# Kernel tuning notes

Hardware: AMD Instinct MI355X
Metric: run time of the kernel (lower is better)

Reference implementation:

```python
import jax, jax.numpy as jnp
import numpy as np

N_NODES = 50000


def setup_inputs() -> dict:
    key = jax.random.key(0)
    ks = jax.random.split(key, 6)
    F_IN, F_HID, N_EDGES = 128, 512, 800000
    x = jax.random.normal(ks[0], (N_NODES, F_IN), dtype=jnp.float32)
    edge_index = jax.random.randint(ks[1], (2, N_EDGES), 0, N_NODES, dtype=jnp.int64)
    W1 = jax.random.normal(ks[2], (F_IN, F_HID), dtype=jnp.float32) * (1.0 / np.sqrt(F_IN))
    b1 = jnp.zeros((F_HID,), dtype=jnp.float32)
    W2 = jax.random.normal(ks[3], (F_HID, F_IN), dtype=jnp.float32) * (1.0 / np.sqrt(F_HID))
    b2 = jnp.zeros((F_IN,), dtype=jnp.float32)
    eps = jnp.zeros((), dtype=jnp.float32)  # train_eps=True, init 0
    return {"x": x, "edge_index": edge_index, "W1": W1, "b1": b1, "W2": W2, "b2": b2, "eps": eps}


def reference(x, edge_index, W1, b1, W2, b2, eps):
    # GINConv: out = MLP((1+eps)*x + sum_{j in N(i)} x_j)
    src, dst = edge_index[0], edge_index[1]
    agg = jax.ops.segment_sum(x[src], dst, num_segments=N_NODES)  # [N, F]
    h = (1.0 + eps) * x + agg
    h = jax.nn.relu(h @ W1 + b1)
    out = h @ W2 + b2
    return out
```

## Files before the change

kernel.cpp:

```cpp
#include <hip/hip_runtime.h>
#include <hip/hip_bf16.h>

#define N_NODES 50000
#define F_IN    128
#define F_HID   512
#define N_EDGES 800000

#define NBKT 782
#define NREP 8
#define RCAP 256
#define NDMAX 64
#define NZERO 50000

typedef __bf16 bf16x2 __attribute__((ext_vector_type(2)));
typedef __bf16 bf16x4 __attribute__((ext_vector_type(4)));
typedef __bf16 bf16x8 __attribute__((ext_vector_type(8)));
typedef float  f32x4  __attribute__((ext_vector_type(4)));
typedef unsigned short u16x8 __attribute__((ext_vector_type(8)));

#define NB_E 782
__global__ __launch_bounds__(256) void fillk(const int* __restrict__ ei,
                                             int* __restrict__ bcnt,
                                             int* __restrict__ entries) {
    int b = blockIdx.x, tid = threadIdx.x;
    int e0 = (b * 256 + tid) * 4;
    int rep = b & (NREP - 1);
    if (e0 + 4 <= N_EDGES) {
        int4 s4 = *(const int4*)&ei[e0];
        int4 d4 = *(const int4*)&ei[N_EDGES + e0];
        int c0 = (d4.x >> 6) * NREP + rep;
        int c1 = (d4.y >> 6) * NREP + rep;
        int c2 = (d4.z >> 6) * NREP + rep;
        int c3 = (d4.w >> 6) * NREP + rep;
        int p0 = atomicAdd(&bcnt[c0 * 16], 1);
        int p1 = atomicAdd(&bcnt[c1 * 16], 1);
        int p2 = atomicAdd(&bcnt[c2 * 16], 1);
        int p3 = atomicAdd(&bcnt[c3 * 16], 1);
        if (p0 < RCAP) entries[(size_t)c0 * RCAP + p0] = ((d4.x & 63) << 16) | s4.x;
        if (p1 < RCAP) entries[(size_t)c1 * RCAP + p1] = ((d4.y & 63) << 16) | s4.y;
        if (p2 < RCAP) entries[(size_t)c2 * RCAP + p2] = ((d4.z & 63) << 16) | s4.z;
        if (p3 < RCAP) entries[(size_t)c3 * RCAP + p3] = ((d4.w & 63) << 16) | s4.w;
    } else {
        for (int k = 0; k < 4; ++k) {
            int e = e0 + k;
            if (e < N_EDGES) {
                int src = ei[e], dst = ei[N_EDGES + e];
                int c = (dst >> 6) * NREP + rep;
                int p = atomicAdd(&bcnt[c * 16], 1);
                if (p < RCAP) entries[(size_t)c * RCAP + p] = ((dst & 63) << 16) | src;
            }
        }
    }
}

#define NB_X 6250
#define NB_W 32
__global__ __launch_bounds__(256) void prep(const float* __restrict__ x,
                                            const float* __restrict__ W1,
                                            const float* __restrict__ W2,
                                            __bf16* __restrict__ xb,
                                            __bf16* __restrict__ w1f,
                                            __bf16* __restrict__ w2f) {
    int b = blockIdx.x, tid = threadIdx.x;
    if (b < NB_X) {
        int i = b * 256 + tid;
        float4 v = ((const float4*)x)[i];
        bf16x4 o = {(__bf16)v.x, (__bf16)v.y, (__bf16)v.z, (__bf16)v.w};
        ((bf16x4*)xb)[i] = o;
    } else if (b < NB_X + NB_W) {
        int t = (b - NB_X) * 256 + tid;
        int lane = t & 63, kk = (t >> 6) & 3, nt = (t >> 8) & 7, c = (t >> 11) & 3;
        int q = lane >> 4, l16 = lane & 15;
        bf16x8 o;
        #pragma unroll
        for (int j = 0; j < 8; ++j)
            o[j] = (__bf16)W1[(kk * 32 + q * 8 + j) * F_HID + c * 128 + nt * 16 + l16];
        *(bf16x8*)(w1f + (size_t)t * 8) = o;
    } else {
        int t = (b - NB_X - NB_W) * 256 + tid;
        int lane = t & 63, kk = (t >> 6) & 3, nt = (t >> 8) & 7, c = (t >> 11) & 3;
        int q = lane >> 4, l16 = lane & 15;
        bf16x8 o;
        #pragma unroll
        for (int j = 0; j < 8; ++j)
            o[j] = (__bf16)W2[(c * 128 + kk * 32 + q * 8 + j) * F_IN + nt * 16 + l16];
        *(bf16x8*)(w2f + (size_t)t * 8) = o;
    }
}

__global__ __launch_bounds__(512) void gin_fused(const __bf16* __restrict__ xb,
                                                 const int* __restrict__ bcnt,
                                                 const int* __restrict__ entries,
                                                 const float* __restrict__ eps,
                                                 const __bf16* __restrict__ w1f,
                                                 const __bf16* __restrict__ w2f,
                                                 const float* __restrict__ b1,
                                                 const float* __restrict__ b2,
                                                 float* __restrict__ out) {
    __shared__ union __attribute__((aligned(16))) {
        struct { int degs[64]; unsigned short bin16[64 * NDMAX]; } p0;
        __bf16 Hb[8192];
    } u;
    __shared__ __attribute__((aligned(16))) __bf16 As[8192];

    const int tid = threadIdx.x;
    const int wave = tid >> 6, lane = tid & 63;
    const int q = lane >> 4, l16 = lane & 15;
    const int bkt = blockIdx.x;

    if (tid < 64) u.p0.degs[tid] = 0;
    {
        const int zz = (NZERO << 16) | NZERO;
        int* b32 = (int*)u.p0.bin16;
        #pragma unroll
        for (int k = 0; k < 4; ++k) b32[tid * 4 + k] = zz;
    }
    __syncthreads();

    {
        int cell = bkt * NREP + wave;
        int cnt = bcnt[cell * 16];
        cnt = cnt < RCAP ? cnt : RCAP;
        const int* eb = entries + (size_t)cell * RCAP;
        for (int i = lane; i < cnt; i += 64) {
            int en = eb[i];
            int dl = en >> 16;
            int p = atomicAdd(&u.p0.degs[dl], 1);
            if (p < NDMAX)
                u.p0.bin16[dl * NDMAX + (p & 3) * 16 + (p >> 2)] =
                    (unsigned short)(en & 0xffff);
        }
    }
    __syncthreads();

    const float s = 1.0f + eps[0];
#define ROW(idx) (*(const bf16x8*)(xb + (size_t)(idx) * F_IN + l16 * 8))
    #pragma unroll 2
    for (int t = 0; t < 8; ++t) {
        int n = wave * 8 + t;
        int node = bkt * 64 + n;
        int dg = u.p0.degs[n];
        dg = dg < NDMAX ? dg : NDMAX;
        int myc = (dg + 3 - q) >> 2;
        u16x8 I0 = *(const u16x8*)&u.p0.bin16[n * NDMAX + q * 16];
        u16x8 I1 = *(const u16x8*)&u.p0.bin16[n * NDMAX + q * 16 + 8];

        float acc[8];
        #pragma unroll
        for (int i = 0; i < 8; ++i) acc[i] = 0.0f;
        if (q == 0) {
            bf16x8 self = ROW(node);
            #pragma unroll
            for (int i = 0; i < 8; ++i) acc[i] = (float)self[i] * s;
        }

        bf16x8 ra0 = ROW(I0[0]), ra1 = ROW(I0[1]), ra2 = ROW(I0[2]), ra3 = ROW(I0[3]);
        bf16x8 rb0 = ROW(I0[4]), rb1 = ROW(I0[5]), rb2 = ROW(I0[6]), rb3 = ROW(I0[7]);
        #pragma unroll
        for (int i = 0; i < 8; ++i)
            acc[i] += ((float)ra0[i] + (float)ra1[i]) + ((float)ra2[i] + (float)ra3[i]);
        #pragma unroll
        for (int i = 0; i < 8; ++i)
            acc[i] += ((float)rb0[i] + (float)rb1[i]) + ((float)rb2[i] + (float)rb3[i]);

        if (myc > 8) {
            #pragma unroll
            for (int v = 0; v < 8; ++v)
                if (myc > 8 + v) {
                    bf16x8 r = ROW(I1[v]);
                    #pragma unroll
                    for (int i = 0; i < 8; ++i) acc[i] += (float)r[i];
                }
        }

        #pragma unroll
        for (int i = 0; i < 8; ++i) {
            acc[i] += __shfl_xor(acc[i], 16);
            acc[i] += __shfl_xor(acc[i], 32);
        }
        if (lane < 16) {
            int g = n >> 4, r16 = n & 15;
            bf16x8 o;
            #pragma unroll
            for (int i = 0; i < 8; ++i) o[i] = (__bf16)acc[i];
            int byte = (g * 16 + lane) * 256 + r16 * 16;
            byte ^= (lane & 7) << 4;
            *(bf16x8*)((char*)As + byte) = o;
        }
    }
    __syncthreads();

    const int wr = wave >> 2, wc = wave & 3;

    f32x4 acc_o[2][2];
    #pragma unroll
    for (int ni = 0; ni < 2; ++ni) {
        float bv = b2[wc * 32 + ni * 16 + l16];
        f32x4 b4 = {bv, bv, bv, bv};
        acc_o[0][ni] = b4;
        acc_o[1][ni] = b4;
    }

    for (int c = 0; c < 4; ++c) {
        f32x4 acc_h[2][2];
        #pragma unroll
        for (int ni = 0; ni < 2; ++ni) {
            float bv = b1[c * 128 + wc * 32 + ni * 16 + l16];
            f32x4 b4 = {bv, bv, bv, bv};
            acc_h[0][ni] = b4;
            acc_h[1][ni] = b4;
        }
        #pragma unroll
        for (int kk = 0; kk < 4; ++kk) {
            bf16x8 am[2], bw[2];
            #pragma unroll
            for (int mi = 0; mi < 2; ++mi) {
                int g = wr * 2 + mi;
                int byte = ((g * 4 + kk) * 4 + q) * 256 + l16 * 16;
                byte ^= ((kk * 4 + q) & 7) << 4;
                am[mi] = *(const bf16x8*)((const char*)As + byte);
            }
            #pragma unroll
            for (int ni = 0; ni < 2; ++ni)
                bw[ni] = *(const bf16x8*)(w1f +
                    ((size_t)((c * 8 + wc * 2 + ni) * 4 + kk) << 9) + lane * 8);
            #pragma unroll
            for (int mi = 0; mi < 2; ++mi)
                #pragma unroll
                for (int ni = 0; ni < 2; ++ni)
                    acc_h[mi][ni] = __builtin_amdgcn_mfma_f32_16x16x32_bf16(
                        am[mi], bw[ni], acc_h[mi][ni], 0, 0, 0);
        }
        #pragma unroll
        for (int mi = 0; mi < 2; ++mi) {
            int g = wr * 2 + mi;
            #pragma unroll
            for (int ni = 0; ni < 2; ++ni)
                #pragma unroll
                for (int r = 0; r < 4; ++r)
                    u.Hb[(((g * 4 + wc) * 64 + (ni * 2 + (l16 >> 3)) * 16 + q * 4 + r) << 3)
                         + (l16 & 7)] = (__bf16)fmaxf(acc_h[mi][ni][r], 0.0f);
        }
        __syncthreads();

        #pragma unroll
        for (int kk = 0; kk < 4; ++kk) {
            bf16x8 am[2], bw[2];
            #pragma unroll
            for (int mi = 0; mi < 2; ++mi)
                am[mi] = *(const bf16x8*)&u.Hb[(((wr * 2 + mi) * 4 + kk) * 64 + lane) << 3];
            #pragma unroll
            for (int ni = 0; ni < 2; ++ni)
                bw[ni] = *(const bf16x8*)(w2f +
                    ((size_t)((c * 8 + wc * 2 + ni) * 4 + kk) << 9) + lane * 8);
            #pragma unroll
            for (int mi = 0; mi < 2; ++mi)
                #pragma unroll
                for (int ni = 0; ni < 2; ++ni)
                    acc_o[mi][ni] = __builtin_amdgcn_mfma_f32_16x16x32_bf16(
                        am[mi], bw[ni], acc_o[mi][ni], 0, 0, 0);
        }
        __syncthreads();
    }

    const int m0 = bkt * 64;
    #pragma unroll
    for (int mi = 0; mi < 2; ++mi)
        #pragma unroll
        for (int ni = 0; ni < 2; ++ni)
            #pragma unroll
            for (int r = 0; r < 4; ++r) {
                int m = m0 + wr * 32 + mi * 16 + q * 4 + r;
                if (m < N_NODES)
                    out[(size_t)m * F_IN + wc * 32 + ni * 16 + l16] = acc_o[mi][ni][r];
            }
}

extern "C" void kernel_launch(void* const* d_in, const int* in_sizes, int n_in,
                              void* d_out, int out_size, void* d_ws, size_t ws_size,
                              hipStream_t stream) {
    const float* x   = (const float*)d_in[0];
    const int*   ei  = (const int*)d_in[1];
    const float* W1  = (const float*)d_in[2];
    const float* b1  = (const float*)d_in[3];
    const float* W2  = (const float*)d_in[4];
    const float* b2  = (const float*)d_in[5];
    const float* eps = (const float*)d_in[6];
    float* out = (float*)d_out;

    char* ws = (char*)d_ws;
    __bf16* xb   = (__bf16*)ws;
    __bf16* w1f  = (__bf16*)(ws + 12900000);
    __bf16* w2f  = (__bf16*)(ws + 13100000);
    int*    bcnt = (int*)(ws + 13300000);
    int*    entries = (int*)(ws + 13800000);

    hipMemsetAsync(bcnt, 0, NBKT * NREP * 64, stream);
    hipMemsetAsync((char*)ws + (size_t)N_NODES * F_IN * 2, 0, 48 * F_IN * 2, stream);
    fillk<<<NB_E, 256, 0, stream>>>(ei, bcnt, entries);
    prep<<<NB_X + 2 * NB_W, 256, 0, stream>>>(x, W1, W2, xb, w1f, w2f);
    gin_fused<<<NBKT, 512, 0, stream>>>(xb, bcnt, entries, eps, w1f, w2f, b1, b2, out);
}
```

Baseline: 187.4 us.

## Merge fill and prep kernels; bucket edges via block-local LDS histogram

The edge-bucketing kernel and the bf16 conversion kernel become one launch with 1024-thread blocks. Each fill block first builds a per-bucket histogram in shared memory, then reserves space with a single global atomic per bucket, which replaces one global atomic per edge and the 8-way replica cells. The main kernel then reads one contiguous bucket of up to 1280 entries per block, spread across all 512 threads. This removes a launch and most of the global atomic contention. The cost is LDS atomics and extra block barriers, plus a capacity cap that could drop edges if a bucket overflows.

```diff
diff --git a/kernel.cpp b/kernel.cpp
--- a/kernel.cpp
+++ b/kernel.cpp
@@ -7,8 +7,7 @@
 #define N_EDGES 800000
 
 #define NBKT 782
-#define NREP 8
-#define RCAP 256
+#define BKCAP 1280
 #define NDMAX 64
 #define NZERO 50000
 
@@ -18,57 +17,62 @@
 typedef float  f32x4  __attribute__((ext_vector_type(4)));
 typedef unsigned short u16x8 __attribute__((ext_vector_type(8)));
 
-#define NB_E 782
-__global__ __launch_bounds__(256) void fillk(const int* __restrict__ ei,
-                                             int* __restrict__ bcnt,
-                                             int* __restrict__ entries) {
+#define NB_F 196
+#define NB_X 1563
+#define NB_W 8
+__global__ __launch_bounds__(1024) void fill_prep(const float* __restrict__ x,
+                                                  const int* __restrict__ ei,
+                                                  const float* __restrict__ W1,
+                                                  const float* __restrict__ W2,
+                                                  __bf16* __restrict__ xb,
+                                                  __bf16* __restrict__ w1f,
+                                                  __bf16* __restrict__ w2f,
+                                                  int* __restrict__ gcnt,
+                                                  int* __restrict__ entries) {
     int b = blockIdx.x, tid = threadIdx.x;
-    int e0 = (b * 256 + tid) * 4;
-    int rep = b & (NREP - 1);
-    if (e0 + 4 <= N_EDGES) {
-        int4 s4 = *(const int4*)&ei[e0];
-        int4 d4 = *(const int4*)&ei[N_EDGES + e0];
-        int c0 = (d4.x >> 6) * NREP + rep;
-        int c1 = (d4.y >> 6) * NREP + rep;
-        int c2 = (d4.z >> 6) * NREP + rep;
-        int c3 = (d4.w >> 6) * NREP + rep;
-        int p0 = atomicAdd(&bcnt[c0 * 16], 1);
-        int p1 = atomicAdd(&bcnt[c1 * 16], 1);
-        int p2 = atomicAdd(&bcnt[c2 * 16], 1);
-        int p3 = atomicAdd(&bcnt[c3 * 16], 1);
-        if (p0 < RCAP) entries[(size_t)c0 * RCAP + p0] = ((d4.x & 63) << 16) | s4.x;
-        if (p1 < RCAP) entries[(size_t)c1 * RCAP + p1] = ((d4.y & 63) << 16) | s4.y;
-        if (p2 < RCAP) entries[(size_t)c2 * RCAP + p2] = ((d4.z & 63) << 16) | s4.z;
-        if (p3 < RCAP) entries[(size_t)c3 * RCAP + p3] = ((d4.w & 63) << 16) | s4.w;
-    } else {
+    if (b < NB_F) {
+        __shared__ int hist[NBKT], base_[NBKT];
+        for (int i = tid; i < NBKT; i += 1024) hist[i] = 0;
+        __syncthreads();
+
+        int e0 = (b * 1024 + tid) * 4;
+        int bk[4], sl[4], pay[4];
+        bool act[4];
+        #pragma unroll
         for (int k = 0; k < 4; ++k) {
             int e = e0 + k;
-            if (e < N_EDGES) {
-                int src = ei[e], dst = ei[N_EDGES + e];
-                int c = (dst >> 6) * NREP + rep;
-                int p = atomicAdd(&bcnt[c * 16], 1);
-                if (p < RCAP) entries[(size_t)c * RCAP + p] = ((dst & 63) << 16) | src;
+            act[k] = (e < N_EDGES);
+            if (act[k]) {
+                int src = ei[e];
+                int dst = ei[N_EDGES + e];
+                bk[k] = dst >> 6;
+                pay[k] = ((dst & 63) << 16) | src;
+                sl[k] = atomicAdd(&hist[bk[k]], 1);
             }
         }
-    }
-}
-
-#define NB_X 6250
-#define NB_W 32
-__global__ __launch_bounds__(256) void prep(const float* __restrict__ x,
-                                            const float* __restrict__ W1,
-                                            const float* __restrict__ W2,
-                                            __bf16* __restrict__ xb,
-                                            __bf16* __restrict__ w1f,
-                                            __bf16* __restrict__ w2f) {
-    int b = blockIdx.x, tid = threadIdx.x;
-    if (b < NB_X) {
-        int i = b * 256 + tid;
-        float4 v = ((const float4*)x)[i];
-        bf16x4 o = {(__bf16)v.x, (__bf16)v.y, (__bf16)v.z, (__bf16)v.w};
-        ((bf16x4*)xb)[i] = o;
-    } else if (b < NB_X + NB_W) {
-        int t = (b - NB_X) * 256 + tid;
+        __syncthreads();
+
+        for (int i = tid; i < NBKT; i += 1024) {
+            int h = hist[i];
+            base_[i] = h ? atomicAdd(&gcnt[i * 16], h) : 0;
+        }
+        __syncthreads();
+
+        #pragma unroll
+        for (int k = 0; k < 4; ++k)
+            if (act[k]) {
+                int p = base_[bk[k]] + sl[k];
+                if (p < BKCAP) entries[(size_t)bk[k] * BKCAP + p] = pay[k];
+            }
+    } else if (b < NB_F + NB_X) {
+        int i = (b - NB_F) * 1024 + tid;
+        if (i < 1600000) {
+            float4 v = ((const float4*)x)[i];
+            bf16x4 o = {(__bf16)v.x, (__bf16)v.y, (__bf16)v.z, (__bf16)v.w};
+            ((bf16x4*)xb)[i] = o;
+        }
+    } else if (b < NB_F + NB_X + NB_W) {
+        int t = (b - NB_F - NB_X) * 1024 + tid;
         int lane = t & 63, kk = (t >> 6) & 3, nt = (t >> 8) & 7, c = (t >> 11) & 3;
         int q = lane >> 4, l16 = lane & 15;
         bf16x8 o;
@@ -77,7 +81,7 @@
             o[j] = (__bf16)W1[(kk * 32 + q * 8 + j) * F_HID + c * 128 + nt * 16 + l16];
         *(bf16x8*)(w1f + (size_t)t * 8) = o;
     } else {
-        int t = (b - NB_X - NB_W) * 256 + tid;
+        int t = (b - NB_F - NB_X - NB_W) * 1024 + tid;
         int lane = t & 63, kk = (t >> 6) & 3, nt = (t >> 8) & 7, c = (t >> 11) & 3;
         int q = lane >> 4, l16 = lane & 15;
         bf16x8 o;
@@ -89,7 +93,7 @@
 }
 
 __global__ __launch_bounds__(512) void gin_fused(const __bf16* __restrict__ xb,
-                                                 const int* __restrict__ bcnt,
+                                                 const int* __restrict__ gcnt,
                                                  const int* __restrict__ entries,
                                                  const float* __restrict__ eps,
                                                  const __bf16* __restrict__ w1f,
@@ -118,11 +122,10 @@
     __syncthreads();
 
     {
-        int cell = bkt * NREP + wave;
-        int cnt = bcnt[cell * 16];
-        cnt = cnt < RCAP ? cnt : RCAP;
-        const int* eb = entries + (size_t)cell * RCAP;
-        for (int i = lane; i < cnt; i += 64) {
+        int cnt = gcnt[bkt * 16];
+        cnt = cnt < BKCAP ? cnt : BKCAP;
+        const int* eb = entries + (size_t)bkt * BKCAP;
+        for (int i = tid; i < cnt; i += 512) {
             int en = eb[i];
             int dl = en >> 16;
             int p = atomicAdd(&u.p0.degs[dl], 1);
@@ -292,12 +295,12 @@
     __bf16* xb   = (__bf16*)ws;
     __bf16* w1f  = (__bf16*)(ws + 12900000);
     __bf16* w2f  = (__bf16*)(ws + 13100000);
-    int*    bcnt = (int*)(ws + 13300000);
-    int*    entries = (int*)(ws + 13800000);
-
-    hipMemsetAsync(bcnt, 0, NBKT * NREP * 64, stream);
+    int*    gcnt = (int*)(ws + 13300000);
+    int*    entries = (int*)(ws + 13400000);
+
+    hipMemsetAsync(gcnt, 0, NBKT * 64, stream);
     hipMemsetAsync((char*)ws + (size_t)N_NODES * F_IN * 2, 0, 48 * F_IN * 2, stream);
-    fillk<<<NB_E, 256, 0, stream>>>(ei, bcnt, entries);
-    prep<<<NB_X + 2 * NB_W, 256, 0, stream>>>(x, W1, W2, xb, w1f, w2f);
-    gin_fused<<<NBKT, 512, 0, stream>>>(xb, bcnt, entries, eps, w1f, w2f, b1, b2, out);
+    fill_prep<<<NB_F + NB_X + 2 * NB_W, 1024, 0, stream>>>(x, ei, W1, W2,
+                                                           xb, w1f, w2f, gcnt, entries);
+    gin_fused<<<NBKT, 512, 0, stream>>>(xb, gcnt, entries, eps, w1f, w2f, b1, b2, out);
 }
```

After: 158.7 us. -15.3%, faster.
